# Optimization experiments

Hardware: AMD Instinct MI355X
Metric: run time of the kernel (lower is better)

The kernel has to match this reference:

```python
import jax, jax.numpy as jnp
import numpy as np

B, S, D_IN, D_OUT, H = 2, 2048, 1024, 1024, 16
DK = D_OUT // H


def setup_inputs() -> dict:
    key = jax.random.key(0)
    ks = jax.random.split(key, 6)
    s_in = 1.0 / np.sqrt(D_IN)
    s_out = 1.0 / np.sqrt(D_OUT)
    return {
        "x": jax.random.normal(ks[0], (B, S, D_IN), dtype=jnp.float32),
        "Wq": jax.random.uniform(ks[1], (D_OUT, D_IN), jnp.float32, -s_in, s_in),
        "Wk": jax.random.uniform(ks[2], (D_OUT, D_IN), jnp.float32, -s_in, s_in),
        "Wv": jax.random.uniform(ks[3], (D_OUT, D_IN), jnp.float32, -s_in, s_in),
        "Wo": jax.random.uniform(ks[4], (D_OUT, D_OUT), jnp.float32, -s_out, s_out),
        "bo": jax.random.uniform(ks[5], (D_OUT,), jnp.float32, -s_out, s_out),
    }


def reference(x, Wq, Wk, Wv, Wo, bo):
    b, s, _ = x.shape
    # torch Linear: y = x @ W.T
    q = (x @ Wq.T).reshape(b, s, H, DK).transpose(0, 2, 1, 3)  # [b,h,s,dk]
    k = (x @ Wk.T).reshape(b, s, H, DK).transpose(0, 2, 1, 3)
    v = (x @ Wv.T).reshape(b, s, H, DK).transpose(0, 2, 1, 3)
    scores = jnp.einsum("bhqd,bhkd->bhqk", q, k)
    causal = jnp.tril(jnp.ones((s, s), dtype=bool))  # True = keep
    scores = jnp.where(causal, scores, -jnp.inf)
    attn = jax.nn.softmax(scores / np.sqrt(DK), axis=-1)
    # dropout p=0.0 (eval) -> identity
    ctx = jnp.einsum("bhqk,bhkd->bhqd", attn, v)
    ctx = ctx.transpose(0, 2, 1, 3).reshape(b, s, D_OUT)
    return ctx @ Wo.T + bo
```

## Files before the change

### kernel.cpp

```cpp
#include <hip/hip_runtime.h>
#include <stdint.h>

#define B_   2
#define S_   2048
#define DIN  1024
#define DOUT 1024
#define H_   16
#define DK_  64
#define MSZ  (B_ * S_)

typedef __bf16 bf16v8 __attribute__((ext_vector_type(8)));
typedef float  f32x4  __attribute__((ext_vector_type(4)));

__device__ __forceinline__ ushort f2b(float f) {
  union { float f; uint32_t u; } a; a.f = f;
  uint32_t u = a.u;
  u += 0x7FFFu + ((u >> 16) & 1u);
  return (ushort)(u >> 16);
}

__device__ __forceinline__ uint32_t pk2(float lo, float hi) {
  union { __bf16 h; ushort u; } a, b;
  a.h = (__bf16)lo; b.h = (__bf16)hi;
  return (uint32_t)a.u | ((uint32_t)b.u << 16);
}

#define GLDS(gp, lp) __builtin_amdgcn_global_load_lds(                         \
    (const __attribute__((address_space(1))) void*)(gp),                       \
    (__attribute__((address_space(3))) void*)(lp), 16, 0, 0)

__global__ void cvt_all(const float* __restrict__ x,  const float* __restrict__ wq,
                        const float* __restrict__ wk, const float* __restrict__ wv,
                        const float* __restrict__ wo,
                        ushort* __restrict__ xb,  ushort* __restrict__ wqb,
                        ushort* __restrict__ wkb, ushort* __restrict__ wvb,
                        ushort* __restrict__ wob) {
  int i = blockIdx.x * blockDim.x + threadIdx.x;
  const int NX = 1 << 20, NW = 1 << 18;
  const float* src; ushort* dst; int off;
  if (i < NX)               { src = x;  dst = xb;  off = i; }
  else if (i < NX + NW)     { src = wq; dst = wqb; off = i - NX; }
  else if (i < NX + 2 * NW) { src = wk; dst = wkb; off = i - NX - NW; }
  else if (i < NX + 3 * NW) { src = wv; dst = wvb; off = i - NX - 2 * NW; }
  else                      { src = wo; dst = wob; off = i - NX - 3 * NW; }
  float4 v = reinterpret_cast<const float4*>(src)[off];
  ushort4 o;
  o.x = f2b(v.x); o.y = f2b(v.y); o.z = f2b(v.z); o.w = f2b(v.w);
  reinterpret_cast<ushort4*>(dst)[off] = o;
}

template<int MODE>
__global__ __launch_bounds__(256)
void gemm_nt(const ushort* __restrict__ A,
             const ushort* __restrict__ Bq, const ushort* __restrict__ Bk,
             const ushort* __restrict__ Bv,
             ushort* __restrict__ Oq, ushort* __restrict__ Ok,
             ushort* __restrict__ Vt,
             float* __restrict__ Cf, const float* __restrict__ bias,
             int M, int K) {
  __shared__ ushort sA[128 * 64];
  __shared__ ushort sB[128 * 64];

  const int tid  = threadIdx.x;
  const int lane = tid & 63, wid = tid >> 6;
  const int wr = wid >> 1, wc = wid & 1;
  const int g = lane >> 4, c = lane & 15;
  const int m0 = blockIdx.x * 128;

  int wsel = 0, n0w = blockIdx.y * 128;
  const ushort* Bm;
  if (MODE == 0) {
    wsel = blockIdx.y >> 3;
    n0w  = (blockIdx.y & 7) * 128;
    Bm = (wsel == 0) ? Bq : (wsel == 1) ? Bk : Bv;
  } else {
    Bm = Bq;
  }

  const int msk = (c & 7) << 4;

  f32x4 acc[4][4] = {};

  for (int k0 = 0; k0 < K; k0 += 64) {
    __syncthreads();
#pragma unroll
    for (int i = 0; i < 4; ++i) {
      int idx = i * 256 + tid;
      int row = idx >> 3;
      int scol = (((idx & 7) ^ (row & 7)) << 3);
      GLDS(A  + (size_t)(m0 + row) * K + k0 + scol,
           (char*)sA + idx * 16);
      GLDS(Bm + (size_t)(n0w + row) * K + k0 + scol,
           (char*)sB + idx * 16);
    }
    __syncthreads();

    bf16v8 aF[4][2], bF[4][2];
#pragma unroll
    for (int m = 0; m < 4; ++m) {
      const char* rp = (const char*)sA + (wr * 64 + m * 16 + c) * 128;
#pragma unroll
      for (int ks = 0; ks < 2; ++ks)
        aF[m][ks] = *reinterpret_cast<const bf16v8*>(rp + ((ks * 64 + g * 16) ^ msk));
    }
#pragma unroll
    for (int n = 0; n < 4; ++n) {
      const char* rp = (const char*)sB + (wc * 64 + n * 16 + c) * 128;
#pragma unroll
      for (int ks = 0; ks < 2; ++ks)
        bF[n][ks] = *reinterpret_cast<const bf16v8*>(rp + ((ks * 64 + g * 16) ^ msk));
    }
#pragma unroll
    for (int m = 0; m < 4; ++m)
#pragma unroll
      for (int n = 0; n < 4; ++n) {
        acc[m][n] = __builtin_amdgcn_mfma_f32_16x16x32_bf16(aF[m][0], bF[n][0], acc[m][n], 0, 0, 0);
        acc[m][n] = __builtin_amdgcn_mfma_f32_16x16x32_bf16(aF[m][1], bF[n][1], acc[m][n], 0, 0, 0);
      }
  }

  __syncthreads();

  if (MODE == 0 && wsel == 2) {
#pragma unroll
    for (int m = 0; m < 4; ++m)
#pragma unroll
      for (int n = 0; n < 4; ++n) {
        int row0 = m0 + wr * 64 + g * 4 + m * 16;
        int col  = n0w + wc * 64 + c + n * 16;
        int bb = row0 >> 11, ss = row0 & 2047;
        int hh = col >> 6, dd = col & 63;
        ushort4 o4;
        o4.x = f2b(acc[m][n][0]); o4.y = f2b(acc[m][n][1]);
        o4.z = f2b(acc[m][n][2]); o4.w = f2b(acc[m][n][3]);
        *reinterpret_cast<ushort4*>(
            &Vt[((size_t)(bb * 16 + hh) * 64 + dd) * 2048 + ss]) = o4;
      }
  } else if (MODE == 0) {
    const float oscale = (wsel == 0) ? 0.125f * 1.4426950408889634f : 1.0f;
    ushort* Ob = (wsel == 0) ? Oq : Ok;
    char* eb = (char*)sA + wid * 2048;
#pragma unroll
    for (int m = 0; m < 4; ++m) {
#pragma unroll
      for (int n = 0; n < 4; ++n)
#pragma unroll
        for (int i = 0; i < 4; ++i) {
          int prow = g * 4 + i;
          *(ushort*)(eb + prow * 128 + ((n * 32 + c * 2) ^ ((prow & 7) << 4))) =
              f2b(acc[m][n][i] * oscale);
        }
      const int r = lane >> 2, cq = lane & 3;
      const int m2 = (r & 7) << 4;
      bf16v8 t0 = *reinterpret_cast<const bf16v8*>(eb + r * 128 + ((cq * 32) ^ m2));
      bf16v8 t1 = *reinterpret_cast<const bf16v8*>(eb + r * 128 + ((cq * 32 + 16) ^ m2));
      ushort* Gb = Ob + (size_t)(m0 + wr * 64 + m * 16 + r) * DOUT +
                   n0w + wc * 64 + cq * 16;
      *reinterpret_cast<bf16v8*>(Gb) = t0;
      *reinterpret_cast<bf16v8*>(Gb + 8) = t1;
    }
  } else {
    float bv[4];
#pragma unroll
    for (int n = 0; n < 4; ++n) bv[n] = bias[n0w + wc * 64 + n * 16 + c];
    float* ef = (float*)((char*)sA + wid * 4096);
#pragma unroll
    for (int m = 0; m < 4; ++m) {
#pragma unroll
      for (int n = 0; n < 4; ++n)
#pragma unroll
        for (int i = 0; i < 4; ++i) {
          int prow = g * 4 + i;
          ef[prow * 64 + ((n * 16 + c) ^ ((prow & 12) << 2))] = acc[m][n][i] + bv[n];
        }
      const int r = lane >> 2, q = lane & 3;
      const int mk = (r & 12) << 2;
#pragma unroll
      for (int k = 0; k < 4; ++k) {
        float4 v = *reinterpret_cast<const float4*>(&ef[r * 64 + ((q * 16 + k * 4) ^ mk)]);
        *reinterpret_cast<float4*>(
            &Cf[(size_t)(m0 + wr * 64 + m * 16 + r) * DOUT +
                n0w + wc * 64 + q * 16 + k * 4]) = v;
      }
    }
  }
}

__global__ __launch_bounds__(512)
void flash_attn(const ushort* __restrict__ Q, const ushort* __restrict__ K,
                const ushort* __restrict__ Vt, ushort* __restrict__ O) {
  __shared__ ushort sK[2][64][64];
  __shared__ ushort sV[2][64][64];
  __shared__ ushort sP[8][16][64];

  const int tid  = threadIdx.x;
  const int lane = tid & 63, wid = tid >> 6;
  const int wid4 = wid & 3;
  const int g = lane >> 4, c = lane & 15;

  const int orig = blockIdx.x;
  const int xcd  = orig & 7, idc = orig >> 3;
  const int bh   = xcd * 4 + (idc >> 4);
  const int tp   = idc & 15;
  const int b = bh >> 4, h = bh & 15;
  const int q0    = (wid < 4) ? tp * 64 : (31 - tp) * 64;
  const int q0max = (31 - tp) * 64;

  const ushort* Qb = Q  + (size_t)b * S_ * DOUT + h * DK_;
  const ushort* Kb = K  + (size_t)b * S_ * DOUT + h * DK_;
  const ushort* Vb = Vt + (size_t)bh * DK_ * S_;

  const int srow = tid >> 3;
  const int swc  = ((tid & 7) ^ (srow & 7)) << 3;
  const int msk  = (c & 7) << 4;
  const int pswz = (c & 7) << 2;

  bf16v8 qf[2];
  {
    const ushort* qrow = Qb + (size_t)(q0 + wid4 * 16 + c) * DOUT;
    qf[0] = *reinterpret_cast<const bf16v8*>(qrow + g * 8);
    qf[1] = *reinterpret_cast<const bf16v8*>(qrow + 32 + g * 8);
  }

  bf16v8 ones;
#pragma unroll
  for (int j = 0; j < 8; ++j) ones[j] = (__bf16)1.0f;

  GLDS(Kb + (size_t)srow * DOUT + swc, (char*)&sK[0][0][0] + tid * 16);
  GLDS(Vb + (size_t)srow * S_  + swc, (char*)&sV[0][0][0] + tid * 16);
  __syncthreads();

  f32x4 accO[4] = {};
  f32x4 accL = {};
  char* sPw = (char*)&sP[wid][0][0];
  const int qg = q0 + wid4 * 16 + c;
  const int qdiag = q0 + wid4 * 16;

  int buf = 0;
  for (int kv0 = 0; kv0 <= q0max; kv0 += 64, buf ^= 1) {
    if (kv0 + 64 <= q0max) {
      const int nb = buf ^ 1, kvn = kv0 + 64;
      GLDS(Kb + (size_t)(kvn + srow) * DOUT + swc,
           (char*)&sK[nb][0][0] + tid * 16);
      GLDS(Vb + (size_t)srow * S_ + kvn + swc,
           (char*)&sV[nb][0][0] + tid * 16);
    }

    if (kv0 <= q0) {
      const char* cK = (const char*)&sK[buf][0][0];
      const char* cV = (const char*)&sV[buf][0][0];

      f32x4 s[4] = {};
      __builtin_amdgcn_s_setprio(1);
#pragma unroll
      for (int nf = 0; nf < 4; ++nf) {
        const char* rp = cK + (nf * 16 + c) * 128;
#pragma unroll
        for (int ks = 0; ks < 2; ++ks) {
          bf16v8 kf = *reinterpret_cast<const bf16v8*>(rp + ((ks * 64 + g * 16) ^ msk));
          s[nf] = __builtin_amdgcn_mfma_f32_16x16x32_bf16(kf, qf[ks], s[nf], 0, 0, 0);
        }
      }
      __builtin_amdgcn_s_setprio(0);

      if (kv0 + 63 > qdiag) {
#pragma unroll
        for (int nf = 0; nf < 4; ++nf)
#pragma unroll
          for (int i = 0; i < 4; ++i)
            if (kv0 + nf * 16 + g * 4 + i > qg) s[nf][i] = -1e30f;
      }

#pragma unroll
      for (int nf = 0; nf < 4; ++nf) {
        float p0 = exp2f(s[nf][0]), p1 = exp2f(s[nf][1]);
        float p2 = exp2f(s[nf][2]), p3 = exp2f(s[nf][3]);
        uint2 w2; w2.x = pk2(p0, p1); w2.y = pk2(p2, p3);
        *reinterpret_cast<uint2*>(
            sPw + c * 128 + (((nf * 8 + g * 2) ^ pswz) << 2)) = w2;
      }
      bf16v8 pf[2];
#pragma unroll
      for (int ks = 0; ks < 2; ++ks)
        pf[ks] = *reinterpret_cast<const bf16v8*>(
            sPw + c * 128 + (((ks * 16 + g * 4) ^ pswz) << 2));

      __builtin_amdgcn_s_setprio(1);
#pragma unroll
      for (int ks = 0; ks < 2; ++ks)
        accL = __builtin_amdgcn_mfma_f32_16x16x32_bf16(pf[ks], ones, accL, 0, 0, 0);
#pragma unroll
      for (int nf2 = 0; nf2 < 4; ++nf2) {
        const char* vp = cV + (nf2 * 16 + c) * 128;
#pragma unroll
        for (int ks = 0; ks < 2; ++ks) {
          bf16v8 vf = *reinterpret_cast<const bf16v8*>(vp + ((ks * 64 + g * 16) ^ msk));
          accO[nf2] = __builtin_amdgcn_mfma_f32_16x16x32_bf16(pf[ks], vf, accO[nf2], 0, 0, 0);
        }
      }
      __builtin_amdgcn_s_setprio(0);
    }

    __syncthreads();
  }

#pragma unroll
  for (int nf = 0; nf < 4; ++nf)
#pragma unroll
    for (int i = 0; i < 4; ++i) {
      int prow = g * 4 + i;
      float v = accO[nf][i] / accL[i];
      *(ushort*)(sPw + prow * 128 +
                 ((nf * 32 + c * 2) ^ ((prow & 7) << 4))) = f2b(v);
    }
  {
    const int r = lane >> 2, cq = lane & 3;
    const char* base = sPw + r * 128;
    const int m2 = (r & 7) << 4;
    bf16v8 t0 = *reinterpret_cast<const bf16v8*>(base + ((cq * 32) ^ m2));
    bf16v8 t1 = *reinterpret_cast<const bf16v8*>(base + ((cq * 32 + 16) ^ m2));
    ushort* Gb = O + (size_t)b * S_ * DOUT +
                 (size_t)(q0 + wid4 * 16 + r) * DOUT + h * DK_ + cq * 16;
    *reinterpret_cast<bf16v8*>(Gb) = t0;
    *reinterpret_cast<bf16v8*>(Gb + 8) = t1;
  }
}

extern "C" void kernel_launch(void* const* d_in, const int* in_sizes, int n_in,
                              void* d_out, int out_size, void* d_ws, size_t ws_size,
                              hipStream_t stream) {
  const float* x  = (const float*)d_in[0];
  const float* Wq = (const float*)d_in[1];
  const float* Wk = (const float*)d_in[2];
  const float* Wv = (const float*)d_in[3];
  const float* Wo = (const float*)d_in[4];
  const float* bo = (const float*)d_in[5];
  float* out = (float*)d_out;

  char* ws = (char*)d_ws;
  const size_t MB = (size_t)1 << 20;
  ushort* xb  = (ushort*)(ws);
  ushort* wqb = (ushort*)(ws +  8 * MB);
  ushort* wkb = (ushort*)(ws + 10 * MB);
  ushort* wvb = (ushort*)(ws + 12 * MB);
  ushort* wob = (ushort*)(ws + 14 * MB);
  ushort* qb  = (ushort*)(ws + 16 * MB);
  ushort* kb  = (ushort*)(ws + 24 * MB);
  ushort* vtb = (ushort*)(ws + 32 * MB);
  ushort* cb  = (ushort*)(ws);

  const int ncv = (1 << 20) + 4 * (1 << 18);
  cvt_all<<<ncv / 256, 256, 0, stream>>>(x, Wq, Wk, Wv, Wo,
                                         xb, wqb, wkb, wvb, wob);

  dim3 gqkv(MSZ / 128, 24, 1);
  gemm_nt<0><<<gqkv, 256, 0, stream>>>(xb, wqb, wkb, wvb, qb, kb, vtb,
                                       nullptr, nullptr, MSZ, DIN);

  flash_attn<<<B_ * H_ * (S_ / 128), 512, 0, stream>>>(qb, kb, vtb, cb);

  dim3 gproj(MSZ / 128, DOUT / 128, 1);
  gemm_nt<1><<<gproj, 256, 0, stream>>>(cb, wob, nullptr, nullptr,
                                        nullptr, nullptr, nullptr, out, bo,
                                        MSZ, DOUT);
}
```

Before: 117.4 us.

## Split projection GEMM into 64x64 tiles and widen attention KV blocks to 128

The output projection moves to its own kernel with 64x64 tiles, which quadruples the grid from 256 to 1024 blocks so the GPU's compute units stay busy. The QKV GEMM becomes a non-templated kernel. Flash attention now loads 128-key K/V tiles per iteration and processes them as two 64-key sub-blocks, which halves the number of barriers and prefetch rounds. The cost is double the LDS for K/V, which may lower occupancy, and the smaller projection tiles reuse each loaded tile less.

```diff
diff --git a/kernel.cpp b/kernel.cpp
--- a/kernel.cpp
+++ b/kernel.cpp
@@ -49,15 +49,12 @@
   reinterpret_cast<ushort4*>(dst)[off] = o;
 }
 
-template<int MODE>
 __global__ __launch_bounds__(256)
-void gemm_nt(const ushort* __restrict__ A,
-             const ushort* __restrict__ Bq, const ushort* __restrict__ Bk,
-             const ushort* __restrict__ Bv,
-             ushort* __restrict__ Oq, ushort* __restrict__ Ok,
-             ushort* __restrict__ Vt,
-             float* __restrict__ Cf, const float* __restrict__ bias,
-             int M, int K) {
+void gemm_qkv(const ushort* __restrict__ A,
+              const ushort* __restrict__ Bq, const ushort* __restrict__ Bk,
+              const ushort* __restrict__ Bv,
+              ushort* __restrict__ Oq, ushort* __restrict__ Ok,
+              ushort* __restrict__ Vt, int M, int K) {
   __shared__ ushort sA[128 * 64];
   __shared__ ushort sB[128 * 64];
 
@@ -67,15 +64,9 @@
   const int g = lane >> 4, c = lane & 15;
   const int m0 = blockIdx.x * 128;
 
-  int wsel = 0, n0w = blockIdx.y * 128;
-  const ushort* Bm;
-  if (MODE == 0) {
-    wsel = blockIdx.y >> 3;
-    n0w  = (blockIdx.y & 7) * 128;
-    Bm = (wsel == 0) ? Bq : (wsel == 1) ? Bk : Bv;
-  } else {
-    Bm = Bq;
-  }
+  const int wsel = blockIdx.y >> 3;
+  const int n0w  = (blockIdx.y & 7) * 128;
+  const ushort* Bm = (wsel == 0) ? Bq : (wsel == 1) ? Bk : Bv;
 
   const int msk = (c & 7) << 4;
 
@@ -88,10 +79,8 @@
       int idx = i * 256 + tid;
       int row = idx >> 3;
       int scol = (((idx & 7) ^ (row & 7)) << 3);
-      GLDS(A  + (size_t)(m0 + row) * K + k0 + scol,
-           (char*)sA + idx * 16);
-      GLDS(Bm + (size_t)(n0w + row) * K + k0 + scol,
-           (char*)sB + idx * 16);
+      GLDS(A  + (size_t)(m0 + row) * K + k0 + scol, (char*)sA + idx * 16);
+      GLDS(Bm + (size_t)(n0w + row) * K + k0 + scol, (char*)sB + idx * 16);
     }
     __syncthreads();
 
@@ -121,7 +110,7 @@
 
   __syncthreads();
 
-  if (MODE == 0 && wsel == 2) {
+  if (wsel == 2) {
 #pragma unroll
     for (int m = 0; m < 4; ++m)
 #pragma unroll
@@ -136,7 +125,7 @@
         *reinterpret_cast<ushort4*>(
             &Vt[((size_t)(bb * 16 + hh) * 64 + dd) * 2048 + ss]) = o4;
       }
-  } else if (MODE == 0) {
+  } else {
     const float oscale = (wsel == 0) ? 0.125f * 1.4426950408889634f : 1.0f;
     ushort* Ob = (wsel == 0) ? Oq : Ok;
     char* eb = (char*)sA + wid * 2048;
@@ -159,38 +148,93 @@
       *reinterpret_cast<bf16v8*>(Gb) = t0;
       *reinterpret_cast<bf16v8*>(Gb + 8) = t1;
     }
-  } else {
-    float bv[4];
-#pragma unroll
-    for (int n = 0; n < 4; ++n) bv[n] = bias[n0w + wc * 64 + n * 16 + c];
-    float* ef = (float*)((char*)sA + wid * 4096);
-#pragma unroll
-    for (int m = 0; m < 4; ++m) {
-#pragma unroll
-      for (int n = 0; n < 4; ++n)
-#pragma unroll
-        for (int i = 0; i < 4; ++i) {
-          int prow = g * 4 + i;
-          ef[prow * 64 + ((n * 16 + c) ^ ((prow & 12) << 2))] = acc[m][n][i] + bv[n];
-        }
-      const int r = lane >> 2, q = lane & 3;
-      const int mk = (r & 12) << 2;
-#pragma unroll
-      for (int k = 0; k < 4; ++k) {
-        float4 v = *reinterpret_cast<const float4*>(&ef[r * 64 + ((q * 16 + k * 4) ^ mk)]);
-        *reinterpret_cast<float4*>(
-            &Cf[(size_t)(m0 + wr * 64 + m * 16 + r) * DOUT +
-                n0w + wc * 64 + q * 16 + k * 4]) = v;
+  }
+}
+
+__global__ __launch_bounds__(256)
+void gemm_proj(const ushort* __restrict__ A, const ushort* __restrict__ Bw,
+               float* __restrict__ Cf, const float* __restrict__ bias,
+               int M, int K) {
+  __shared__ ushort sAB[2][64 * 64];
+
+  const int tid  = threadIdx.x;
+  const int lane = tid & 63, wid = tid >> 6;
+  const int wr = wid >> 1, wc = wid & 1;
+  const int g = lane >> 4, c = lane & 15;
+  const int m0 = blockIdx.x * 64, n0 = blockIdx.y * 64;
+
+  const int msk = (c & 7) << 4;
+
+  f32x4 acc[2][2] = {};
+
+  for (int k0 = 0; k0 < K; k0 += 64) {
+    __syncthreads();
+#pragma unroll
+    for (int i = 0; i < 2; ++i) {
+      int idx = i * 256 + tid;
+      int row = idx >> 3;
+      int scol = (((idx & 7) ^ (row & 7)) << 3);
+      GLDS(A  + (size_t)(m0 + row) * K + k0 + scol, (char*)&sAB[0][0] + idx * 16);
+      GLDS(Bw + (size_t)(n0 + row) * K + k0 + scol, (char*)&sAB[1][0] + idx * 16);
+    }
+    __syncthreads();
+
+    bf16v8 aF[2][2], bF[2][2];
+#pragma unroll
+    for (int m = 0; m < 2; ++m) {
+      const char* rp = (const char*)&sAB[0][0] + (wr * 32 + m * 16 + c) * 128;
+#pragma unroll
+      for (int ks = 0; ks < 2; ++ks)
+        aF[m][ks] = *reinterpret_cast<const bf16v8*>(rp + ((ks * 64 + g * 16) ^ msk));
+    }
+#pragma unroll
+    for (int n = 0; n < 2; ++n) {
+      const char* rp = (const char*)&sAB[1][0] + (wc * 32 + n * 16 + c) * 128;
+#pragma unroll
+      for (int ks = 0; ks < 2; ++ks)
+        bF[n][ks] = *reinterpret_cast<const bf16v8*>(rp + ((ks * 64 + g * 16) ^ msk));
+    }
+#pragma unroll
+    for (int m = 0; m < 2; ++m)
+#pragma unroll
+      for (int n = 0; n < 2; ++n) {
+        acc[m][n] = __builtin_amdgcn_mfma_f32_16x16x32_bf16(aF[m][0], bF[n][0], acc[m][n], 0, 0, 0);
+        acc[m][n] = __builtin_amdgcn_mfma_f32_16x16x32_bf16(aF[m][1], bF[n][1], acc[m][n], 0, 0, 0);
       }
-    }
+  }
+
+  __syncthreads();
+
+  float bv[2];
+#pragma unroll
+  for (int n = 0; n < 2; ++n) bv[n] = bias[n0 + wc * 32 + n * 16 + c];
+
+  float* ef = (float*)((char*)&sAB[0][0] + wid * 4096);
+#pragma unroll
+  for (int m = 0; m < 2; ++m)
+#pragma unroll
+    for (int n = 0; n < 2; ++n)
+#pragma unroll
+      for (int i = 0; i < 4; ++i) {
+        int row = m * 16 + g * 4 + i;
+        ef[row * 32 + ((n * 16 + c) ^ ((row & 7) << 2))] = acc[m][n][i] + bv[n];
+      }
+#pragma unroll
+  for (int pass = 0; pass < 4; ++pass) {
+    int idx = pass * 64 + lane;
+    int row = idx >> 3, q = idx & 7;
+    float4 v = *reinterpret_cast<const float4*>(
+        &ef[row * 32 + ((q * 4) ^ ((row & 7) << 2))]);
+    *reinterpret_cast<float4*>(
+        &Cf[(size_t)(m0 + wr * 32 + row) * DOUT + n0 + wc * 32 + q * 4]) = v;
   }
 }
 
 __global__ __launch_bounds__(512)
 void flash_attn(const ushort* __restrict__ Q, const ushort* __restrict__ K,
                 const ushort* __restrict__ Vt, ushort* __restrict__ O) {
-  __shared__ ushort sK[2][64][64];
-  __shared__ ushort sV[2][64][64];
+  __shared__ ushort sK[2][128][64];
+  __shared__ ushort sV[2][64][128];
   __shared__ ushort sP[8][16][64];
 
   const int tid  = threadIdx.x;
@@ -210,10 +254,15 @@
   const ushort* Kb = K  + (size_t)b * S_ * DOUT + h * DK_;
   const ushort* Vb = Vt + (size_t)bh * DK_ * S_;
 
-  const int srow = tid >> 3;
-  const int swc  = ((tid & 7) ^ (srow & 7)) << 3;
   const int msk  = (c & 7) << 4;
   const int pswz = (c & 7) << 2;
+
+  const int kr0 = tid >> 3,        kc0 = ((tid & 7) ^ (kr0 & 7)) << 3;
+  const int kr1 = (tid + 512) >> 3, kc1 = (((tid + 512) & 7) ^ (kr1 & 7)) << 3;
+  const int vd0 = tid >> 4,        vh0 = (tid >> 3) & 1;
+  const int vc0 = ((tid & 7) ^ (vd0 & 7)) << 3;
+  const int vd1 = (tid + 512) >> 4, vh1 = ((tid + 512) >> 3) & 1;
+  const int vc1 = (((tid + 512) & 7) ^ (vd1 & 7)) << 3;
 
   bf16v8 qf[2];
   {
@@ -226,8 +275,10 @@
 #pragma unroll
   for (int j = 0; j < 8; ++j) ones[j] = (__bf16)1.0f;
 
-  GLDS(Kb + (size_t)srow * DOUT + swc, (char*)&sK[0][0][0] + tid * 16);
-  GLDS(Vb + (size_t)srow * S_  + swc, (char*)&sV[0][0][0] + tid * 16);
+  GLDS(Kb + (size_t)kr0 * DOUT + kc0, (char*)&sK[0][0][0] + tid * 16);
+  GLDS(Kb + (size_t)kr1 * DOUT + kc1, (char*)&sK[0][0][0] + (tid + 512) * 16);
+  GLDS(Vb + (size_t)vd0 * S_ + vh0 * 64 + vc0, (char*)&sV[0][0][0] + tid * 16);
+  GLDS(Vb + (size_t)vd1 * S_ + vh1 * 64 + vc1, (char*)&sV[0][0][0] + (tid + 512) * 16);
   __syncthreads();
 
   f32x4 accO[4] = {};
@@ -237,68 +288,72 @@
   const int qdiag = q0 + wid4 * 16;
 
   int buf = 0;
-  for (int kv0 = 0; kv0 <= q0max; kv0 += 64, buf ^= 1) {
-    if (kv0 + 64 <= q0max) {
-      const int nb = buf ^ 1, kvn = kv0 + 64;
-      GLDS(Kb + (size_t)(kvn + srow) * DOUT + swc,
-           (char*)&sK[nb][0][0] + tid * 16);
-      GLDS(Vb + (size_t)srow * S_ + kvn + swc,
-           (char*)&sV[nb][0][0] + tid * 16);
-    }
-
-    if (kv0 <= q0) {
-      const char* cK = (const char*)&sK[buf][0][0];
-      const char* cV = (const char*)&sV[buf][0][0];
-
-      f32x4 s[4] = {};
-      __builtin_amdgcn_s_setprio(1);
-#pragma unroll
-      for (int nf = 0; nf < 4; ++nf) {
-        const char* rp = cK + (nf * 16 + c) * 128;
-#pragma unroll
-        for (int ks = 0; ks < 2; ++ks) {
-          bf16v8 kf = *reinterpret_cast<const bf16v8*>(rp + ((ks * 64 + g * 16) ^ msk));
-          s[nf] = __builtin_amdgcn_mfma_f32_16x16x32_bf16(kf, qf[ks], s[nf], 0, 0, 0);
+  for (int kv0 = 0; kv0 <= q0max; kv0 += 128, buf ^= 1) {
+    if (kv0 + 128 <= q0max) {
+      const int nb = buf ^ 1, kvn = kv0 + 128;
+      GLDS(Kb + (size_t)(kvn + kr0) * DOUT + kc0, (char*)&sK[nb][0][0] + tid * 16);
+      GLDS(Kb + (size_t)(kvn + kr1) * DOUT + kc1, (char*)&sK[nb][0][0] + (tid + 512) * 16);
+      GLDS(Vb + (size_t)vd0 * S_ + kvn + vh0 * 64 + vc0, (char*)&sV[nb][0][0] + tid * 16);
+      GLDS(Vb + (size_t)vd1 * S_ + kvn + vh1 * 64 + vc1, (char*)&sV[nb][0][0] + (tid + 512) * 16);
+    }
+
+#pragma unroll
+    for (int sub = 0; sub < 2; ++sub) {
+      const int kvs = kv0 + sub * 64;
+      if (kvs <= q0) {
+        const char* cK = (const char*)&sK[buf][0][0] + sub * (64 * 128);
+        const char* cV = (const char*)&sV[buf][0][0] + sub * 128;
+
+        f32x4 s[4] = {};
+        __builtin_amdgcn_s_setprio(1);
+#pragma unroll
+        for (int nf = 0; nf < 4; ++nf) {
+          const char* rp = cK + (nf * 16 + c) * 128;
+#pragma unroll
+          for (int ks = 0; ks < 2; ++ks) {
+            bf16v8 kf = *reinterpret_cast<const bf16v8*>(rp + ((ks * 64 + g * 16) ^ msk));
+            s[nf] = __builtin_amdgcn_mfma_f32_16x16x32_bf16(kf, qf[ks], s[nf], 0, 0, 0);
+          }
         }
+        __builtin_amdgcn_s_setprio(0);
+
+        if (kvs + 63 > qdiag) {
+#pragma unroll
+          for (int nf = 0; nf < 4; ++nf)
+#pragma unroll
+            for (int i = 0; i < 4; ++i)
+              if (kvs + nf * 16 + g * 4 + i > qg) s[nf][i] = -1e30f;
+        }
+
+#pragma unroll
+        for (int nf = 0; nf < 4; ++nf) {
+          float p0 = exp2f(s[nf][0]), p1 = exp2f(s[nf][1]);
+          float p2 = exp2f(s[nf][2]), p3 = exp2f(s[nf][3]);
+          uint2 w2; w2.x = pk2(p0, p1); w2.y = pk2(p2, p3);
+          *reinterpret_cast<uint2*>(
+              sPw + c * 128 + (((nf * 8 + g * 2) ^ pswz) << 2)) = w2;
+        }
+        bf16v8 pf[2];
+#pragma unroll
+        for (int ks = 0; ks < 2; ++ks)
+          pf[ks] = *reinterpret_cast<const bf16v8*>(
+              sPw + c * 128 + (((ks * 16 + g * 4) ^ pswz) << 2));
+
+        __builtin_amdgcn_s_setprio(1);
+#pragma unroll
+        for (int ks = 0; ks < 2; ++ks)
+          accL = __builtin_amdgcn_mfma_f32_16x16x32_bf16(pf[ks], ones, accL, 0, 0, 0);
+#pragma unroll
+        for (int nf2 = 0; nf2 < 4; ++nf2) {
+          const char* vp = cV + (nf2 * 16 + c) * 256;
+#pragma unroll
+          for (int ks = 0; ks < 2; ++ks) {
+            bf16v8 vf = *reinterpret_cast<const bf16v8*>(vp + ((ks * 64 + g * 16) ^ msk));
+            accO[nf2] = __builtin_amdgcn_mfma_f32_16x16x32_bf16(pf[ks], vf, accO[nf2], 0, 0, 0);
+          }
+        }
+        __builtin_amdgcn_s_setprio(0);
       }
-      __builtin_amdgcn_s_setprio(0);
-
-      if (kv0 + 63 > qdiag) {
-#pragma unroll
-        for (int nf = 0; nf < 4; ++nf)
-#pragma unroll
-          for (int i = 0; i < 4; ++i)
-            if (kv0 + nf * 16 + g * 4 + i > qg) s[nf][i] = -1e30f;
-      }
-
-#pragma unroll
-      for (int nf = 0; nf < 4; ++nf) {
-        float p0 = exp2f(s[nf][0]), p1 = exp2f(s[nf][1]);
-        float p2 = exp2f(s[nf][2]), p3 = exp2f(s[nf][3]);
-        uint2 w2; w2.x = pk2(p0, p1); w2.y = pk2(p2, p3);
-        *reinterpret_cast<uint2*>(
-            sPw + c * 128 + (((nf * 8 + g * 2) ^ pswz) << 2)) = w2;
-      }
-      bf16v8 pf[2];
-#pragma unroll
-      for (int ks = 0; ks < 2; ++ks)
-        pf[ks] = *reinterpret_cast<const bf16v8*>(
-            sPw + c * 128 + (((ks * 16 + g * 4) ^ pswz) << 2));
-
-      __builtin_amdgcn_s_setprio(1);
-#pragma unroll
-      for (int ks = 0; ks < 2; ++ks)
-        accL = __builtin_amdgcn_mfma_f32_16x16x32_bf16(pf[ks], ones, accL, 0, 0, 0);
-#pragma unroll
-      for (int nf2 = 0; nf2 < 4; ++nf2) {
-        const char* vp = cV + (nf2 * 16 + c) * 128;
-#pragma unroll
-        for (int ks = 0; ks < 2; ++ks) {
-          bf16v8 vf = *reinterpret_cast<const bf16v8*>(vp + ((ks * 64 + g * 16) ^ msk));
-          accO[nf2] = __builtin_amdgcn_mfma_f32_16x16x32_bf16(pf[ks], vf, accO[nf2], 0, 0, 0);
-        }
-      }
-      __builtin_amdgcn_s_setprio(0);
     }
 
     __syncthreads();
@@ -354,13 +409,11 @@
                                          xb, wqb, wkb, wvb, wob);
 
   dim3 gqkv(MSZ / 128, 24, 1);
-  gemm_nt<0><<<gqkv, 256, 0, stream>>>(xb, wqb, wkb, wvb, qb, kb, vtb,
-                                       nullptr, nullptr, MSZ, DIN);
+  gemm_qkv<<<gqkv, 256, 0, stream>>>(xb, wqb, wkb, wvb, qb, kb, vtb,
+                                     MSZ, DIN);
 
   flash_attn<<<B_ * H_ * (S_ / 128), 512, 0, stream>>>(qb, kb, vtb, cb);
 
-  dim3 gproj(MSZ / 128, DOUT / 128, 1);
-  gemm_nt<1><<<gproj, 256, 0, stream>>>(cb, wob, nullptr, nullptr,
-                                        nullptr, nullptr, nullptr, out, bo,
-                                        MSZ, DOUT);
-}
+  dim3 gproj(MSZ / 64, DOUT / 64, 1);
+  gemm_proj<<<gproj, 256, 0, stream>>>(cb, wob, out, bo, MSZ, DOUT);
+}
```

Result: faster. 107.2 us (-8.7%).
